# Performance work log

Hardware: AMD Instinct MI355X
Metric: run time of the kernel (lower is better)

## Reference

```python
import jax, jax.numpy as jnp
import numpy as np
import math

FACTOR = 1

def setup_inputs() -> dict:
    key = jax.random.key(0)
    k1, k2, k3 = jax.random.split(key, 3)
    B, L, H, E = 32, 1024, 8, 64
    return {
        "queries": jax.random.normal(k1, (B, L, H, E), dtype=jnp.float32),
        "keys": jax.random.normal(k2, (B, L, H, E), dtype=jnp.float32),
        "values": jax.random.normal(k3, (B, L, H, E), dtype=jnp.float32),
        "attn_mask": 0,
    }


def reference(queries, keys, values, attn_mask):
    # queries/keys/values: [B, L, H, E] (S == L so no pad/truncate needed)
    B, L, H, E = queries.shape
    q = jnp.transpose(queries, (0, 2, 3, 1))  # [B,H,E,L]
    k = jnp.transpose(keys, (0, 2, 3, 1))
    v = jnp.transpose(values, (0, 2, 3, 1))   # [B,H,D,L]

    # FFT cross-correlation
    q_fft = jnp.fft.rfft(q, axis=-1)
    k_fft = jnp.fft.rfft(k, axis=-1)
    corr = jnp.fft.irfft(q_fft * jnp.conj(k_fft), n=L, axis=-1)  # [B,H,E,L]

    # top-k delay selection (global over batch, as in source)
    top_k = min(int(FACTOR * math.log(L)), L // 4, 32)  # static: 6
    mean_value = corr.mean(axis=(1, 2))                 # [B,L]
    weights, indices = jax.lax.top_k(mean_value.mean(axis=0), top_k)  # [k]
    tmp_corr = jax.nn.softmax(weights)                  # [k]

    # weighted circular-shift aggregation: roll(v, -indices[i]) summed with tmp_corr[i]
    pos = (jnp.arange(L)[None, :] + indices[:, None]) % L  # [k,L]
    patterns = v[:, :, :, pos]                              # [B,H,D,k,L]
    delays_agg = jnp.einsum('k,bhdkl->bhdl', tmp_corr, patterns)

    return jnp.transpose(delays_agg, (0, 3, 1, 2))  # [B,L,H,D]
```

## Files before the change

kernel.cpp:

```cpp
#include <hip/hip_runtime.h>
#include <math.h>

#define L_SEQ 1024
#define TOPK 6
#define SSTR 1057

#define FFTSTAGE(M, H, SH)                                                \
  _Pragma("unroll")                                                       \
  for (int k_ = 0; k_ < 32; k_ += (M)) {                                  \
    _Pragma("unroll")                                                     \
    for (int t_ = 0; t_ < (H); ++t_) {                                    \
      const float2 w_ = twc[t_ << (SH)];                                  \
      const int a_ = k_ + t_, b_ = a_ + (H);                              \
      const float vr_ = zr[b_] * w_.x - zi[b_] * w_.y;                    \
      const float vi_ = zr[b_] * w_.y + zi[b_] * w_.x;                    \
      zr[b_] = zr[a_] - vr_; zi[b_] = zi[a_] - vi_;                       \
      zr[a_] += vr_;         zi[a_] += vi_;                               \
    }                                                                     \
  }

__global__ __launch_bounds__(256) void fft_spec_kernel(
    const float* __restrict__ q, const float* __restrict__ k,
    float* __restrict__ partial)
{
  __shared__ float pr[8 * SSTR];
  __shared__ float pim[8 * SSTR];
  __shared__ float2 twc[1024];

  const int tid = threadIdx.x;

  const int bid  = blockIdx.x;
  const int work = (bid & 7) * 256 + (bid >> 3);
  const int e0 = (work & 7) * 8;
  const int h  = (work >> 3) & 7;
  const int b  = work >> 6;

  #pragma unroll
  for (int u = 0; u < 4; ++u) {
    const int m = u * 256 + tid;
    float s_, c_;
    sincosf((float)m * 6.13592315e-03f, &s_, &c_);
    twc[m] = make_float2(c_, -s_);
  }

  {
    const float* qb = q + (size_t)b * 524288 + h * 64 + e0;
    const float* kb = k + (size_t)b * 524288 + h * 64 + e0;
    const int ep = (tid & 3) * 2;
    const int lb = tid >> 2;
    #pragma unroll
    for (int it = 0; it < 16; ++it) {
      const int l = it * 64 + lb;
      const float2 qv = *(const float2*)(qb + l * 512 + ep);
      const float2 kv = *(const float2*)(kb + l * 512 + ep);
      const int col = (l & 31) * 33 + (l >> 5);
      pr[(ep + 0) * SSTR + col] = qv.x;
      pr[(ep + 1) * SSTR + col] = qv.y;
      pim[(ep + 0) * SSTR + col] = kv.x;
      pim[(ep + 1) * SSTR + col] = kv.y;
    }
  }
  __syncthreads();

  const int s = tid >> 5;
  const int i = tid & 31;
  const int BR[32] = {0,16,8,24,4,20,12,28,2,18,10,26,6,22,14,30,
                      1,17,9,25,5,21,13,29,3,19,11,27,7,23,15,31};
  float zr[32], zi[32];

  {
    const int rowbase = s * SSTR + i * 33;
    #pragma unroll
    for (int p = 0; p < 32; ++p) {
      zr[p] = pr[rowbase + BR[p]];
      zi[p] = pim[rowbase + BR[p]];
    }
    FFTSTAGE(2, 1, 9) FFTSTAGE(4, 2, 8) FFTSTAGE(8, 4, 7)
    FFTSTAGE(16, 8, 6) FFTSTAGE(32, 16, 5)
    const float2 wstep = twc[i];
    float wr = 1.f, wi = 0.f;
    #pragma unroll
    for (int k2 = 0; k2 < 32; ++k2) {
      pr[rowbase + k2]  = zr[k2] * wr - zi[k2] * wi;
      pim[rowbase + k2] = zr[k2] * wi + zi[k2] * wr;
      const float nwr = wr * wstep.x - wi * wstep.y;
      wi = wr * wstep.y + wi * wstep.x;
      wr = nwr;
    }
  }
  __syncthreads();

  const int j = i;
  #pragma unroll
  for (int p = 0; p < 32; ++p) {
    zr[p] = pr[s * SSTR + BR[p] * 33 + j];
    zi[p] = pim[s * SSTR + BR[p] * 33 + j];
  }
  __syncthreads();
  FFTSTAGE(2, 1, 9) FFTSTAGE(4, 2, 8) FFTSTAGE(8, 4, 7)
  FFTSTAGE(16, 8, 6) FFTSTAGE(32, 16, 5)
  #pragma unroll
  for (int k1 = 0; k1 < 32; ++k1) {
    pr[s * SSTR + j * 33 + k1]  = zr[k1];
    pim[s * SSTR + j * 33 + k1] = zi[k1];
  }
  __syncthreads();

  {
    const int prow = (32 - j) & 31;
    #pragma unroll
    for (int k1 = 0; k1 < 32; ++k1) {
      const int pcol = j ? (31 - k1) : ((32 - k1) & 31);
      const float prr = pr[s * SSTR + prow * 33 + pcol];
      const float pii = pim[s * SSTR + prow * 33 + pcol];
      const float ar = zr[k1], ai = zi[k1];
      zr[k1] = 0.5f * (ar * pii + ai * prr);
      zi[k1] = 0.25f * (ar * ar + ai * ai - prr * prr - pii * pii);
    }
  }
  __syncthreads();
  #pragma unroll
  for (int k1 = 0; k1 < 32; ++k1) {
    pr[s * SSTR + j * 33 + k1]  = zr[k1];
    pim[s * SSTR + j * 33 + k1] = zi[k1];
  }
  __syncthreads();

  #pragma unroll
  for (int u = 0; u < 4; ++u) {
    const int bin = u * 256 + tid;
    const int jj = bin & 31, kk = bin >> 5;
    float sr = 0.f, si = 0.f;
    #pragma unroll
    for (int s2 = 0; s2 < 8; ++s2) {
      sr += pr[s2 * SSTR + jj * 33 + kk];
      si += pim[s2 * SSTR + jj * 33 + kk];
    }
    partial[(size_t)bid * 2048 + bin] = sr;
    partial[(size_t)bid * 2048 + 1024 + bin] = si;
  }
}

__global__ __launch_bounds__(256) void spec_reduce_a(
    const float* __restrict__ partial, float* __restrict__ partial2)
{
  const int v = (blockIdx.x & 7) * 256 + threadIdx.x;
  const int rc = blockIdx.x >> 3;
  float acc = 0.f;
  #pragma unroll 8
  for (int r = rc * 256; r < rc * 256 + 256; ++r)
    acc += partial[(size_t)r * 2048 + v];
  partial2[(size_t)rc * 2048 + v] = acc;
}

__global__ __launch_bounds__(256) void spec_reduce_b(
    const float* __restrict__ partial2, float* __restrict__ S)
{
  const int v = blockIdx.x * 256 + threadIdx.x;
  float acc = 0.f;
  #pragma unroll
  for (int rc = 0; rc < 8; ++rc) acc += partial2[(size_t)rc * 2048 + v];
  S[v] = acc;
}

__global__ __launch_bounds__(256) void corr_kernel(
    const float* __restrict__ S, float* __restrict__ c)
{
  __shared__ float2 twc[1024];
  __shared__ float sm[256];
  const int t = threadIdx.x;
  #pragma unroll
  for (int u = 0; u < 4; ++u) {
    const int m = u * 256 + t;
    float s_, c_;
    sincosf((float)m * 6.13592315e-03f, &s_, &c_);
    twc[m] = make_float2(c_, -s_);
  }
  __syncthreads();
  const int tau = blockIdx.x * 64 + (t & 63);
  const int jc = t >> 6;
  float acc = 0.f;
  for (int jj = 0; jj < 256; ++jj) {
    const int j = jc * 256 + jj;
    const float2 w = twc[(j * tau) & 1023];
    acc += S[j] * w.x + S[1024 + j] * w.y;
  }
  sm[t] = acc;
  __syncthreads();
  if (t < 64)
    c[blockIdx.x * 64 + t] =
        (sm[t] + sm[64 + t] + sm[128 + t] + sm[192 + t]) * (1.0f / 16777216.0f);
}

__global__ __launch_bounds__(256) void topk_kernel(
    const float* __restrict__ c, int* __restrict__ idx_out,
    float* __restrict__ w_out)
{
  __shared__ float vals[L_SEQ];
  __shared__ float rv[256];
  __shared__ int ri[256];
  __shared__ float topv[TOPK];
  __shared__ int topi[TOPK];
  const int tid = threadIdx.x;
  for (int i = tid; i < L_SEQ; i += 256) vals[i] = c[i];
  __syncthreads();

  for (int kk = 0; kk < TOPK; ++kk) {
    float bv = -INFINITY;
    int bi = 1 << 30;
    for (int i = tid; i < L_SEQ; i += 256) {
      const float v = vals[i];
      if (v > bv || (v == bv && i < bi)) { bv = v; bi = i; }
    }
    rv[tid] = bv; ri[tid] = bi;
    __syncthreads();
    for (int off = 128; off > 0; off >>= 1) {
      if (tid < off) {
        const float v2 = rv[tid + off];
        const int i2 = ri[tid + off];
        if (v2 > rv[tid] || (v2 == rv[tid] && i2 < ri[tid])) {
          rv[tid] = v2; ri[tid] = i2;
        }
      }
      __syncthreads();
    }
    if (tid == 0) {
      topv[kk] = rv[0];
      topi[kk] = ri[0];
      vals[ri[0]] = -INFINITY;
    }
    __syncthreads();
  }

  if (tid == 0) {
    const float m = topv[0];
    float e[TOPK], sum = 0.f;
    for (int i = 0; i < TOPK; ++i) { e[i] = expf(topv[i] - m); sum += e[i]; }
    const float inv = 1.0f / sum;
    for (int i = 0; i < TOPK; ++i) { w_out[i] = e[i] * inv; idx_out[i] = topi[i]; }
  }
}

__global__ __launch_bounds__(256) void agg_kernel(
    const float* __restrict__ v, const int* __restrict__ idx,
    const float* __restrict__ w, float4* __restrict__ out)
{
  __shared__ int sidx[TOPK];
  __shared__ float sw[TOPK];
  if (threadIdx.x < TOPK) {
    sidx[threadIdx.x] = idx[threadIdx.x];
    sw[threadIdx.x] = w[threadIdx.x];
  }
  __syncthreads();

  const int i = blockIdx.x * 256 + threadIdx.x;
  const int he4 = i & 127;
  const int l = (i >> 7) & (L_SEQ - 1);
  const int b = i >> 17;
  const float4* vb = (const float4*)v + (size_t)b * (L_SEQ * 128);

  float4 acc = make_float4(0.f, 0.f, 0.f, 0.f);
  #pragma unroll
  for (int kk = 0; kk < TOPK; ++kk) {
    const int src = (l + sidx[kk]) & (L_SEQ - 1);
    const float4 vv = vb[(size_t)src * 128 + he4];
    const float wk = sw[kk];
    acc.x += wk * vv.x; acc.y += wk * vv.y;
    acc.z += wk * vv.z; acc.w += wk * vv.w;
  }
  out[i] = acc;
}

extern "C" void kernel_launch(void* const* d_in, const int* in_sizes, int n_in,
                              void* d_out, int out_size, void* d_ws, size_t ws_size,
                              hipStream_t stream) {
  const float* q = (const float*)d_in[0];
  const float* k = (const float*)d_in[1];
  const float* v = (const float*)d_in[2];

  float* out = (float*)d_out;
  float* partial  = out;
  float* partial2 = out + (size_t)2048 * 2048;

  float* c    = (float*)d_ws;
  int*   idxp = (int*)((char*)d_ws + 4096);
  float* wp   = (float*)((char*)d_ws + 4096 + 64);
  float* S    = (float*)((char*)d_ws + 8192);

  fft_spec_kernel<<<2048, 256, 0, stream>>>(q, k, partial);
  spec_reduce_a<<<64, 256, 0, stream>>>(partial, partial2);
  spec_reduce_b<<<8, 256, 0, stream>>>(partial2, S);
  corr_kernel<<<16, 256, 0, stream>>>(S, c);
  topk_kernel<<<1, 256, 0, stream>>>(c, idxp, wp);
  agg_kernel<<<(L_SEQ * 32 * 128) / 256, 256, 0, stream>>>(v, idxp, wp,
                                                           (float4*)out);
}
```

Baseline: 128.3 us.

## Process four e-chunks per FFT block, constant twiddles, merged spectrum reduction

Each FFT block now loops over four 8-column chunks and accumulates the spectrum in registers, so 512 blocks write partials instead of 2048. The per-block shared twiddle table is gone: the 32-point butterflies use compile-time constants with trivial cases special-cased, and the inter-stage twiddles and correlation DFT use fast __sincosf. The two reduction kernels become one, and the correlation kernel is re-split over 32 blocks. This cuts partial-buffer traffic, sincos setup and one launch, but adds serial work per block, fewer blocks for latency hiding, and slightly less accurate fast sincos.

Result: slower. 173.4 us (+35.2%).

```diff
diff --git a/kernel.cpp b/kernel.cpp
--- a/kernel.cpp
+++ b/kernel.cpp
@@ -4,192 +4,212 @@
 #define L_SEQ 1024
 #define TOPK 6
 #define SSTR 1057
+#define NFBLK 512
+
+__device__ constexpr float TW32R[16] = {
+  1.f, 0.98078528f, 0.92387953f, 0.83146961f, 0.70710678f, 0.55557023f,
+  0.38268343f, 0.19509032f, 0.f, -0.19509032f, -0.38268343f, -0.55557023f,
+  -0.70710678f, -0.83146961f, -0.92387953f, -0.98078528f};
+__device__ constexpr float TW32I[16] = {
+  0.f, -0.19509032f, -0.38268343f, -0.55557023f, -0.70710678f, -0.83146961f,
+  -0.92387953f, -0.98078528f, -1.f, -0.98078528f, -0.92387953f, -0.83146961f,
+  -0.70710678f, -0.55557023f, -0.38268343f, -0.19509032f};
 
 #define FFTSTAGE(M, H, SH)                                                \
   _Pragma("unroll")                                                       \
   for (int k_ = 0; k_ < 32; k_ += (M)) {                                  \
     _Pragma("unroll")                                                     \
     for (int t_ = 0; t_ < (H); ++t_) {                                    \
-      const float2 w_ = twc[t_ << (SH)];                                  \
       const int a_ = k_ + t_, b_ = a_ + (H);                              \
-      const float vr_ = zr[b_] * w_.x - zi[b_] * w_.y;                    \
-      const float vi_ = zr[b_] * w_.y + zi[b_] * w_.x;                    \
+      const int m_ = t_ << (SH);                                          \
+      float vr_, vi_;                                                     \
+      if (m_ == 0)      { vr_ = zr[b_]; vi_ = zi[b_]; }                   \
+      else if (m_ == 8) { vr_ = zi[b_]; vi_ = -zr[b_]; }                  \
+      else {                                                              \
+        vr_ = zr[b_] * TW32R[m_] - zi[b_] * TW32I[m_];                    \
+        vi_ = zr[b_] * TW32I[m_] + zi[b_] * TW32R[m_];                    \
+      }                                                                   \
       zr[b_] = zr[a_] - vr_; zi[b_] = zi[a_] - vi_;                       \
       zr[a_] += vr_;         zi[a_] += vi_;                               \
     }                                                                     \
   }
 
-__global__ __launch_bounds__(256) void fft_spec_kernel(
+__global__ __launch_bounds__(256, 4) void fft_spec_kernel(
     const float* __restrict__ q, const float* __restrict__ k,
     float* __restrict__ partial)
 {
   __shared__ float pr[8 * SSTR];
   __shared__ float pim[8 * SSTR];
-  __shared__ float2 twc[1024];
 
   const int tid = threadIdx.x;
 
-  const int bid  = blockIdx.x;
-  const int work = (bid & 7) * 256 + (bid >> 3);
-  const int e0 = (work & 7) * 8;
-  const int h  = (work >> 3) & 7;
-  const int b  = work >> 6;
-
-  #pragma unroll
-  for (int u = 0; u < 4; ++u) {
-    const int m = u * 256 + tid;
-    float s_, c_;
-    sincosf((float)m * 6.13592315e-03f, &s_, &c_);
-    twc[m] = make_float2(c_, -s_);
-  }
-
-  {
-    const float* qb = q + (size_t)b * 524288 + h * 64 + e0;
-    const float* kb = k + (size_t)b * 524288 + h * 64 + e0;
-    const int ep = (tid & 3) * 2;
-    const int lb = tid >> 2;
-    #pragma unroll
-    for (int it = 0; it < 16; ++it) {
-      const int l = it * 64 + lb;
-      const float2 qv = *(const float2*)(qb + l * 512 + ep);
-      const float2 kv = *(const float2*)(kb + l * 512 + ep);
-      const int col = (l & 31) * 33 + (l >> 5);
+  const int bid   = blockIdx.x;
+  const int work  = (bid & 7) * 64 + (bid >> 3);
+  const int ehalf = work & 1;
+  const int h     = (work >> 1) & 7;
+  const int b     = work >> 4;
+
+  const int s = tid >> 5;
+  const int i = tid & 31;
+  constexpr int BR[32] = {0,16,8,24,4,20,12,28,2,18,10,26,6,22,14,30,
+                          1,17,9,25,5,21,13,29,3,19,11,27,7,23,15,31};
+
+  const float astep = (float)i * 6.13592315e-03f;
+
+  const float* qb = q + (size_t)b * 524288 + h * 64 + ehalf * 32;
+  const float* kb = k + (size_t)b * 524288 + h * 64 + ehalf * 32;
+
+  const int ep  = (tid & 1) * 4;
+  const int lb  = tid >> 1;
+  const int col0 = (lb & 31) * 33 + (lb >> 5);
+
+  float srac[4] = {0.f, 0.f, 0.f, 0.f};
+  float siac[4] = {0.f, 0.f, 0.f, 0.f};
+  float zr[32], zi[32];
+
+  for (int ch = 0; ch < 4; ++ch) {
+    const int e0 = ch * 8;
+
+    __syncthreads();
+    #pragma unroll
+    for (int it = 0; it < 8; ++it) {
+      const int l = it * 128 + lb;
+      const float4 qv = *(const float4*)(qb + l * 512 + e0 + ep);
+      const float4 kv = *(const float4*)(kb + l * 512 + e0 + ep);
+      const int col = col0 + it * 4;
       pr[(ep + 0) * SSTR + col] = qv.x;
       pr[(ep + 1) * SSTR + col] = qv.y;
+      pr[(ep + 2) * SSTR + col] = qv.z;
+      pr[(ep + 3) * SSTR + col] = qv.w;
       pim[(ep + 0) * SSTR + col] = kv.x;
       pim[(ep + 1) * SSTR + col] = kv.y;
-    }
-  }
-  __syncthreads();
-
-  const int s = tid >> 5;
-  const int i = tid & 31;
-  const int BR[32] = {0,16,8,24,4,20,12,28,2,18,10,26,6,22,14,30,
-                      1,17,9,25,5,21,13,29,3,19,11,27,7,23,15,31};
-  float zr[32], zi[32];
-
-  {
-    const int rowbase = s * SSTR + i * 33;
+      pim[(ep + 2) * SSTR + col] = kv.z;
+      pim[(ep + 3) * SSTR + col] = kv.w;
+    }
+    __syncthreads();
+
+    {
+      const int rowbase = s * SSTR + i * 33;
+      #pragma unroll
+      for (int p = 0; p < 32; ++p) {
+        zr[p] = pr[rowbase + BR[p]];
+        zi[p] = pim[rowbase + BR[p]];
+      }
+      FFTSTAGE(2, 1, 4) FFTSTAGE(4, 2, 3) FFTSTAGE(8, 4, 2)
+      FFTSTAGE(16, 8, 1) FFTSTAGE(32, 16, 0)
+      #pragma unroll
+      for (int k2 = 0; k2 < 32; ++k2) {
+        if (k2 == 0) {
+          pr[rowbase]  = zr[0];
+          pim[rowbase] = zi[0];
+        } else {
+          float sa, ca;
+          __sincosf(astep * (float)k2, &sa, &ca);
+          pr[rowbase + k2]  = zr[k2] * ca + zi[k2] * sa;
+          pim[rowbase + k2] = zi[k2] * ca - zr[k2] * sa;
+        }
+      }
+    }
+    __syncthreads();
+
+    const int j = i;
     #pragma unroll
     for (int p = 0; p < 32; ++p) {
-      zr[p] = pr[rowbase + BR[p]];
-      zi[p] = pim[rowbase + BR[p]];
-    }
-    FFTSTAGE(2, 1, 9) FFTSTAGE(4, 2, 8) FFTSTAGE(8, 4, 7)
-    FFTSTAGE(16, 8, 6) FFTSTAGE(32, 16, 5)
-    const float2 wstep = twc[i];
-    float wr = 1.f, wi = 0.f;
-    #pragma unroll
-    for (int k2 = 0; k2 < 32; ++k2) {
-      pr[rowbase + k2]  = zr[k2] * wr - zi[k2] * wi;
-      pim[rowbase + k2] = zr[k2] * wi + zi[k2] * wr;
-      const float nwr = wr * wstep.x - wi * wstep.y;
-      wi = wr * wstep.y + wi * wstep.x;
-      wr = nwr;
-    }
-  }
-  __syncthreads();
-
-  const int j = i;
-  #pragma unroll
-  for (int p = 0; p < 32; ++p) {
-    zr[p] = pr[s * SSTR + BR[p] * 33 + j];
-    zi[p] = pim[s * SSTR + BR[p] * 33 + j];
-  }
-  __syncthreads();
-  FFTSTAGE(2, 1, 9) FFTSTAGE(4, 2, 8) FFTSTAGE(8, 4, 7)
-  FFTSTAGE(16, 8, 6) FFTSTAGE(32, 16, 5)
-  #pragma unroll
-  for (int k1 = 0; k1 < 32; ++k1) {
-    pr[s * SSTR + j * 33 + k1]  = zr[k1];
-    pim[s * SSTR + j * 33 + k1] = zi[k1];
-  }
-  __syncthreads();
-
-  {
-    const int prow = (32 - j) & 31;
+      zr[p] = pr[s * SSTR + BR[p] * 33 + j];
+      zi[p] = pim[s * SSTR + BR[p] * 33 + j];
+    }
+    __syncthreads();
+    FFTSTAGE(2, 1, 4) FFTSTAGE(4, 2, 3) FFTSTAGE(8, 4, 2)
+    FFTSTAGE(16, 8, 1) FFTSTAGE(32, 16, 0)
     #pragma unroll
     for (int k1 = 0; k1 < 32; ++k1) {
-      const int pcol = j ? (31 - k1) : ((32 - k1) & 31);
-      const float prr = pr[s * SSTR + prow * 33 + pcol];
-      const float pii = pim[s * SSTR + prow * 33 + pcol];
-      const float ar = zr[k1], ai = zi[k1];
-      zr[k1] = 0.5f * (ar * pii + ai * prr);
-      zi[k1] = 0.25f * (ar * ar + ai * ai - prr * prr - pii * pii);
-    }
-  }
-  __syncthreads();
-  #pragma unroll
-  for (int k1 = 0; k1 < 32; ++k1) {
-    pr[s * SSTR + j * 33 + k1]  = zr[k1];
-    pim[s * SSTR + j * 33 + k1] = zi[k1];
-  }
-  __syncthreads();
+      pr[s * SSTR + j * 33 + k1]  = zr[k1];
+      pim[s * SSTR + j * 33 + k1] = zi[k1];
+    }
+    __syncthreads();
+
+    {
+      const int prow = (32 - j) & 31;
+      #pragma unroll
+      for (int k1 = 0; k1 < 32; ++k1) {
+        const int pcol = j ? (31 - k1) : ((32 - k1) & 31);
+        const float prr = pr[s * SSTR + prow * 33 + pcol];
+        const float pii = pim[s * SSTR + prow * 33 + pcol];
+        const float ar = zr[k1], ai = zi[k1];
+        zr[k1] = 0.5f * (ar * pii + ai * prr);
+        zi[k1] = 0.25f * (ar * ar + ai * ai - prr * prr - pii * pii);
+      }
+    }
+    __syncthreads();
+    #pragma unroll
+    for (int k1 = 0; k1 < 32; ++k1) {
+      pr[s * SSTR + j * 33 + k1]  = zr[k1];
+      pim[s * SSTR + j * 33 + k1] = zi[k1];
+    }
+    __syncthreads();
+
+    #pragma unroll
+    for (int u = 0; u < 4; ++u) {
+      const int bin = u * 256 + tid;
+      const int jj = bin & 31, kk = bin >> 5;
+      float sr = 0.f, si = 0.f;
+      #pragma unroll
+      for (int s2 = 0; s2 < 8; ++s2) {
+        sr += pr[s2 * SSTR + jj * 33 + kk];
+        si += pim[s2 * SSTR + jj * 33 + kk];
+      }
+      srac[u] += sr;
+      siac[u] += si;
+    }
+  }
 
   #pragma unroll
   for (int u = 0; u < 4; ++u) {
     const int bin = u * 256 + tid;
-    const int jj = bin & 31, kk = bin >> 5;
-    float sr = 0.f, si = 0.f;
-    #pragma unroll
-    for (int s2 = 0; s2 < 8; ++s2) {
-      sr += pr[s2 * SSTR + jj * 33 + kk];
-      si += pim[s2 * SSTR + jj * 33 + kk];
-    }
-    partial[(size_t)bid * 2048 + bin] = sr;
-    partial[(size_t)bid * 2048 + 1024 + bin] = si;
-  }
-}
-
-__global__ __launch_bounds__(256) void spec_reduce_a(
-    const float* __restrict__ partial, float* __restrict__ partial2)
-{
-  const int v = (blockIdx.x & 7) * 256 + threadIdx.x;
-  const int rc = blockIdx.x >> 3;
+    partial[(size_t)bid * 2048 + bin]        = srac[u];
+    partial[(size_t)bid * 2048 + 1024 + bin] = siac[u];
+  }
+}
+
+__global__ __launch_bounds__(256) void spec_reduce(
+    const float* __restrict__ partial, float* __restrict__ S)
+{
+  const int t = threadIdx.x;
+  const int b64 = t & 63, rc = t >> 6;
+  const int v = blockIdx.x * 64 + b64;
   float acc = 0.f;
-  #pragma unroll 8
-  for (int r = rc * 256; r < rc * 256 + 256; ++r)
-    acc += partial[(size_t)r * 2048 + v];
-  partial2[(size_t)rc * 2048 + v] = acc;
-}
-
-__global__ __launch_bounds__(256) void spec_reduce_b(
-    const float* __restrict__ partial2, float* __restrict__ S)
-{
-  const int v = blockIdx.x * 256 + threadIdx.x;
-  float acc = 0.f;
-  #pragma unroll
-  for (int rc = 0; rc < 8; ++rc) acc += partial2[(size_t)rc * 2048 + v];
-  S[v] = acc;
+  for (int rr = rc * 128; rr < rc * 128 + 128; ++rr)
+    acc += partial[(size_t)rr * 2048 + v];
+  __shared__ float sm[4][65];
+  sm[rc][b64] = acc;
+  __syncthreads();
+  if (t < 64)
+    S[v] = sm[0][t] + sm[1][t] + sm[2][t] + sm[3][t];
 }
 
 __global__ __launch_bounds__(256) void corr_kernel(
     const float* __restrict__ S, float* __restrict__ c)
 {
-  __shared__ float2 twc[1024];
-  __shared__ float sm[256];
+  __shared__ float sm[8][33];
   const int t = threadIdx.x;
-  #pragma unroll
-  for (int u = 0; u < 4; ++u) {
-    const int m = u * 256 + t;
+  const int tau = blockIdx.x * 32 + (t & 31);
+  const int jc = t >> 5;
+  float acc = 0.f;
+  #pragma unroll 4
+  for (int jj = 0; jj < 128; ++jj) {
+    const int j = jc * 128 + jj;
     float s_, c_;
-    sincosf((float)m * 6.13592315e-03f, &s_, &c_);
-    twc[m] = make_float2(c_, -s_);
-  }
+    __sincosf((float)((j * tau) & 1023) * 6.13592315e-03f, &s_, &c_);
+    acc += S[j] * c_ - S[1024 + j] * s_;
+  }
+  sm[jc][t & 31] = acc;
   __syncthreads();
-  const int tau = blockIdx.x * 64 + (t & 63);
-  const int jc = t >> 6;
-  float acc = 0.f;
-  for (int jj = 0; jj < 256; ++jj) {
-    const int j = jc * 256 + jj;
-    const float2 w = twc[(j * tau) & 1023];
-    acc += S[j] * w.x + S[1024 + j] * w.y;
-  }
-  sm[t] = acc;
-  __syncthreads();
-  if (t < 64)
-    c[blockIdx.x * 64 + t] =
-        (sm[t] + sm[64 + t] + sm[128 + t] + sm[192 + t]) * (1.0f / 16777216.0f);
+  if (t < 32) {
+    float r = 0.f;
+    #pragma unroll
+    for (int g = 0; g < 8; ++g) r += sm[g][t];
+    c[blockIdx.x * 32 + t] = r * (1.0f / 16777216.0f);
+  }
 }
 
 __global__ __launch_bounds__(256) void topk_kernel(
@@ -279,18 +299,16 @@
   const float* v = (const float*)d_in[2];
 
   float* out = (float*)d_out;
-  float* partial  = out;
-  float* partial2 = out + (size_t)2048 * 2048;
+  float* partial = out;
 
   float* c    = (float*)d_ws;
   int*   idxp = (int*)((char*)d_ws + 4096);
   float* wp   = (float*)((char*)d_ws + 4096 + 64);
   float* S    = (float*)((char*)d_ws + 8192);
 
-  fft_spec_kernel<<<2048, 256, 0, stream>>>(q, k, partial);
-  spec_reduce_a<<<64, 256, 0, stream>>>(partial, partial2);
-  spec_reduce_b<<<8, 256, 0, stream>>>(partial2, S);
-  corr_kernel<<<16, 256, 0, stream>>>(S, c);
+  fft_spec_kernel<<<NFBLK, 256, 0, stream>>>(q, k, partial);
+  spec_reduce<<<32, 256, 0, stream>>>(partial, S);
+  corr_kernel<<<32, 256, 0, stream>>>(S, c);
   topk_kernel<<<1, 256, 0, stream>>>(c, idxp, wp);
   agg_kernel<<<(L_SEQ * 32 * 128) / 256, 256, 0, stream>>>(v, idxp, wp,
                                                            (float4*)out);
```
